# Optimization experiments

Hardware: AMD Instinct MI355X
Metric: run time of the kernel (lower is better)

## Reference

```python
import jax, jax.numpy as jnp
import numpy as np
from jax import lax

EPS = 1e-5
GROUPS = 16

def _conv(x, w, b):
    # x: [N,C,H,W], w: [O,I,3,3]
    y = lax.conv_general_dilated(x, w, (1, 1), 'SAME',
                                 dimension_numbers=('NCHW', 'OIHW', 'NCHW'))
    return y + b[None, :, None, None]

def _group_norm(x, gamma, beta):
    N, C, H, W = x.shape
    xr = x.reshape(N, GROUPS, C // GROUPS, H, W)
    m = xr.mean(axis=(2, 3, 4), keepdims=True)
    v = xr.var(axis=(2, 3, 4), keepdims=True)
    xn = ((xr - m) * lax.rsqrt(v + EPS)).reshape(N, C, H, W)
    return xn * gamma[None, :, None, None] + beta[None, :, None, None]

def _tower(x, ws, bs, gs, betas):
    for w, b, g, bt in zip(ws, bs, gs, betas):
        x = jax.nn.relu(_group_norm(_conv(x, w, b), g, bt))
    return x

def _fcos_heads(feats, cls_w, cls_b, cls_g, cls_bt, cls_ow, cls_ob,
                reg_w, reg_b, reg_g, reg_bt, reg_ow, reg_ob, ctr_w, ctr_b):
    outs = []
    for f in feats:
        N = f.shape[0]
        c = _tower(f, cls_w, cls_b, cls_g, cls_bt)
        logits = _conv(c, cls_ow, cls_ob)                 # [N, num_classes, H, W]
        r = _tower(f, reg_w, reg_b, reg_g, reg_bt)
        bbox = jax.nn.relu(_conv(r, reg_ow, reg_ob))      # [N, 4, H, W]
        ctr = _conv(r, ctr_w, ctr_b)                      # [N, 1, H, W]
        lvl = jnp.concatenate([logits, bbox, ctr], axis=1)  # [N, num_classes+5, H, W]
        outs.append(lvl.reshape(N, lvl.shape[1], -1))
    return jnp.concatenate(outs, axis=-1)  # [N, num_classes+5, sum(H*W)]

def setup_inputs() -> dict:
    key = jax.random.key(0)
    C, NUM_CLASSES, NB = 256, 80, 2
    sizes = [(128, 128), (64, 64), (32, 32), (16, 16), (8, 8)]
    keys = iter(jax.random.split(key, 64))
    d = {}
    for i, (h, w) in enumerate(sizes):
        d[f'feat{i}'] = jax.random.normal(next(keys), (NB, C, h, w), jnp.float32)
    for head in ('cls', 'reg'):
        for i in range(3):
            d[f'{head}_w{i}'] = 0.01 * jax.random.normal(next(keys), (C, C, 3, 3), jnp.float32)
            d[f'{head}_b{i}'] = jnp.zeros((C,), jnp.float32)
            d[f'{head}_gn_g{i}'] = jnp.ones((C,), jnp.float32)
            d[f'{head}_gn_b{i}'] = jnp.zeros((C,), jnp.float32)
    d['cls_out_w'] = 0.01 * jax.random.normal(next(keys), (NUM_CLASSES, C, 3, 3), jnp.float32)
    prior = 0.01
    d['cls_out_b'] = jnp.full((NUM_CLASSES,), float(-np.log((1 - prior) / prior)), jnp.float32)
    d['reg_out_w'] = 0.01 * jax.random.normal(next(keys), (4, C, 3, 3), jnp.float32)
    d['reg_out_b'] = jnp.zeros((4,), jnp.float32)
    d['ctr_w'] = 0.01 * jax.random.normal(next(keys), (1, C, 3, 3), jnp.float32)
    d['ctr_b'] = jnp.zeros((1,), jnp.float32)
    return d

def reference(feat0, feat1, feat2, feat3, feat4,
              cls_w0, cls_b0, cls_gn_g0, cls_gn_b0,
              cls_w1, cls_b1, cls_gn_g1, cls_gn_b1,
              cls_w2, cls_b2, cls_gn_g2, cls_gn_b2,
              reg_w0, reg_b0, reg_gn_g0, reg_gn_b0,
              reg_w1, reg_b1, reg_gn_g1, reg_gn_b1,
              reg_w2, reg_b2, reg_gn_g2, reg_gn_b2,
              cls_out_w, cls_out_b, reg_out_w, reg_out_b, ctr_w, ctr_b):
    feats = [feat0, feat1, feat2, feat3, feat4]
    return _fcos_heads(feats,
                       [cls_w0, cls_w1, cls_w2], [cls_b0, cls_b1, cls_b2],
                       [cls_gn_g0, cls_gn_g1, cls_gn_g2], [cls_gn_b0, cls_gn_b1, cls_gn_b2],
                       cls_out_w, cls_out_b,
                       [reg_w0, reg_w1, reg_w2], [reg_b0, reg_b1, reg_b2],
                       [reg_gn_g0, reg_gn_g1, reg_gn_g2], [reg_gn_b0, reg_gn_b1, reg_gn_b2],
                       reg_out_w, reg_out_b, ctr_w, ctr_b)
```

## Files before the change

### kernel.cpp

```cpp
#include <hip/hip_runtime.h>
#include <stdint.h>


typedef __attribute__((ext_vector_type(8))) short short8;
typedef __attribute__((ext_vector_type(4))) float floatx4;

#define XP 349184
#define TIB (32 * XP)

__device__ __forceinline__ unsigned short f2bf(float f) {
  unsigned u = __float_as_uint(f);
  u = (u + 0x7FFFu + ((u >> 16) & 1u)) >> 16;
  return (unsigned short)u;
}
__device__ __forceinline__ unsigned pk2(float a, float b) {
  return (unsigned)f2bf(a) | ((unsigned)f2bf(b) << 16);
}
__device__ __forceinline__ void async16(const void* g, void* l) {
  __builtin_amdgcn_global_load_lds(
      (const __attribute__((address_space(1))) unsigned int*)g,
      (__attribute__((address_space(3))) unsigned int*)l, 16, 0, 0);
}

#define WAIT_VM4 0x0F74
#define WAIT_VM0 0x0F70

__device__ const int d_lw[5]   = {7, 6, 5, 4, 3};
__device__ const int d_off[5]  = {0, 16384, 20480, 21504, 21760};
__device__ const int d_nt[5]   = {128, 32, 8, 2, 1};
__device__ const int d_cumT[6] = {0, 1024, 1280, 1344, 1360, 1368};
__device__ const int d_cumO[6] = {0, 512, 640, 672, 680, 684};
__device__ const int d_cumS[6] = {0, 256, 320, 336, 340, 341};
__device__ const int ck_lvl[13] = {0,0,0,0,0,0,0,0,1,1,2,3,4};
__device__ const int ck_c0[13]  = {0,2048,4096,6144,8192,10240,12288,14336,0,2048,0,0,0};
__device__ const int ck_len[13] = {2048,2048,2048,2048,2048,2048,2048,2048,2048,2048,1024,256,64};

__global__ __launch_bounds__(256) void wtrans(
    const float* __restrict__ c0, const float* __restrict__ c1, const float* __restrict__ c2,
    const float* __restrict__ r0, const float* __restrict__ r1, const float* __restrict__ r2,
    const float* __restrict__ cw, const float* __restrict__ rw, const float* __restrict__ tw,
    unsigned short* __restrict__ dst, float* __restrict__ zp, float* __restrict__ stats) {
  const int z = blockIdx.y;
  if (z == 8) {
    if (blockIdx.x == 0) {
      for (int i = threadIdx.x; i < 384; i += 256) zp[i] = 0.f;
      for (int i = threadIdx.x; i < 1920; i += 256) stats[i] = 0.f;
    }
    return;
  }
  const int nel = (z < 6) ? 589824 : 294912;
  const int idx = blockIdx.x * 256 + threadIdx.x;
  if (idx >= nel) return;
  int tmp = idx;
  const int j = tmp & 7;   tmp >>= 3;
  const int m = tmp & 127; tmp >>= 7;
  const int cs = tmp & 3;  tmp >>= 2;
  const int t = tmp % 9;   tmp /= 9;
  const int cc = tmp & 7;  const int mt = tmp >> 3;
  const int o = mt * 128 + m;
  const int i = cc * 32 + cs * 8 + j;
  float v = 0.f;
  const float* srcs[6] = {c0, c1, c2, r0, r1, r2};
  if (z < 6)      v = srcs[z][((size_t)o * 256 + i) * 9 + t];
  else if (z == 6){ if (o < 80) v = cw[((size_t)o * 256 + i) * 9 + t]; }
  else            { if (o < 4)  v = rw[((size_t)o * 256 + i) * 9 + t];
                    else if (o == 4) v = tw[(size_t)i * 9 + t]; }
  const size_t base = (z < 6) ? (size_t)z * 589824
                              : (size_t)6 * 589824 + (size_t)(z - 6) * 294912;
  dst[base + idx] = f2bf(v);
}

__global__ __launch_bounds__(256) void feat_nhwc(
    const float* __restrict__ s0, const float* __restrict__ s1,
    const float* __restrict__ s2, const float* __restrict__ s3,
    const float* __restrict__ s4, unsigned short* __restrict__ dst) {
  __shared__ unsigned short tile[64][65];
  int bx = blockIdx.x, lvl = 0;
  while (bx >= d_cumS[lvl + 1]) ++lvl;
  const int HW = 1 << (2 * d_lw[lvl]), off = d_off[lvl];
  const float* srcs[5] = {s0, s1, s2, s3, s4};
  const float* src = srcs[lvl];
  const int img = blockIdx.z, c0 = blockIdx.y * 64, p0 = (bx - d_cumS[lvl]) * 64;
  const float* s = src + ((size_t)img * 256 + c0) * HW + p0;
  const int tid = threadIdx.x;
#pragma unroll
  for (int i = 0; i < 4; i++) {
    const int cl = (tid >> 4) + i * 16, pl = (tid & 15) * 4;
    const float4 v = *(const float4*)(s + (size_t)cl * HW + pl);
    tile[cl][pl]     = f2bf(v.x);
    tile[cl][pl + 1] = f2bf(v.y);
    tile[cl][pl + 2] = f2bf(v.z);
    tile[cl][pl + 3] = f2bf(v.w);
  }
  __syncthreads();
  const int pl = tid >> 2, cseg = (tid & 3) * 16;
  unsigned ro[8];
#pragma unroll
  for (int k = 0; k < 8; k++)
    ro[k] = (unsigned)tile[cseg + 2 * k][pl] | ((unsigned)tile[cseg + 2 * k + 1][pl] << 16);
  const int ch0 = c0 + cseg;
  char* db = (char*)dst + (size_t)img * TIB + (size_t)(ch0 >> 3) * XP
           + (size_t)(off + p0 + pl) * 16;
  uint4 u0 = {ro[0], ro[1], ro[2], ro[3]};
  uint4 u1 = {ro[4], ro[5], ro[6], ro[7]};
  *(uint4*)db = u0;
  *(uint4*)(db + XP) = u1;
}

__global__ __launch_bounds__(256) void conv_mfma(
    const unsigned short* __restrict__ xin0, const unsigned short* __restrict__ xin1,
    const unsigned short* __restrict__ wA, const unsigned short* __restrict__ wB,
    unsigned short* __restrict__ y0, unsigned short* __restrict__ y1,
    const float* __restrict__ cb0, const float* __restrict__ cb1,
    float* __restrict__ out,
    const float* __restrict__ ob_cls, const float* __restrict__ ob_reg, const float* __restrict__ ob_ctr,
    const unsigned short* __restrict__ zp, int mode) {
  __shared__ __align__(16) char smem[49152];
  const int tid = threadIdx.x;
  const int* cum = (mode == 0) ? d_cumT : d_cumO;
  const int nwg = (mode == 0) ? 1368 : 684;
  const int xcd = blockIdx.x & 7, cidx = blockIdx.x >> 3;
  const int qq = nwg >> 3, rr = nwg & 7;
  int bid = (xcd < rr ? xcd * (qq + 1) : rr * (qq + 1) + (xcd - rr) * qq) + cidx;
  int lvl = 0;
  while (bid >= cum[lvl + 1]) ++lvl;
  int r = bid - cum[lvl];
  const int lw = d_lw[lvl], W = 1 << lw, HW = 1 << (2 * lw), poffl = d_off[lvl];
  const int ntc = d_nt[lvl];
  const int nt = r % ntc; r /= ntc;
  int mt = 0;
  if (mode == 0) { mt = r & 1; r >>= 1; }
  const int img = r & 1, tower = r >> 1;

  const unsigned short* xin = (tower ? xin1 : xin0) + (size_t)img * 21824 * 256;
  const unsigned short* wset = tower ? wB : wA;

  const int n = tid & 127;
  const int p = nt * 128 + n;
  const bool pv = p < HW;
  const int h = p >> lw, w = p & (W - 1);
  const int kq = tid >> 7;

  const char* xb = (const char*)xin;
  const char* tb[9];
  int stp[9];
#pragma unroll
  for (int t = 0; t < 9; t++) {
    const int rr2 = h + t / 3 - 1, cx = w + t % 3 - 1;
    const bool v = pv && rr2 >= 0 && rr2 < W && cx >= 0 && cx < W;
    tb[t] = v ? xb + (size_t)kq * XP + (size_t)(poffl + rr2 * W + cx) * 16
              : (const char*)zp;
    stp[t] = v ? 4 * XP : 0;
  }

  const char* abase = (const char*)wset + (size_t)mt * 589824;
  const char* a_tid = abase + (size_t)tid * 16;
  char* l_tid = smem + tid * 16;

  const int lane = tid & 63, q = lane >> 4, lr = lane & 15;
  const int wv = tid >> 6, wm = wv >> 1, wn = wv & 1;
  int aoff[4], boff[4];
#pragma unroll
  for (int i = 0; i < 4; i++) {
    aoff[i] = ((q << 7) + wm * 64 + i * 16 + lr) << 4;
    boff[i] = (((q << 7) + wn * 64 + i * 16 + lr) << 4) + 8192;
  }

  floatx4 acc[4][4];
#pragma unroll
  for (int i = 0; i < 4; i++)
#pragma unroll
    for (int j = 0; j < 4; j++) acc[i][j] = (floatx4){0.f, 0.f, 0.f, 0.f};

#define UNIT(CC, U, WIMM)                                                     \
  {                                                                           \
    const int it_ = (CC) * 9 + (U);                                           \
    __builtin_amdgcn_s_waitcnt(WIMM);                                         \
    __builtin_amdgcn_s_barrier();                                             \
    asm volatile("" ::: "memory");                                            \
    if (it_ + 2 < 72) {                                                       \
      const int nu_ = (U) + 2;                                                \
      const int tn_ = nu_ % 9;                              \
      const int ccn_ = (CC) + nu_ / 9;                                        \
      char* la_ = l_tid + (nu_ % 3) * 16384;                                  \
      const char* ap_ = a_tid + (size_t)(it_ + 2) * 8192;                     \
      async16(ap_, la_);                                                      \
      async16(ap_ + 4096, la_ + 4096);                                        \
      const int sp_ = stp[tn_];                                               \
      const char* bp_ = tb[tn_] + ccn_ * sp_;                                 \
      async16(bp_, la_ + 8192);                                               \
      async16(bp_ + (sp_ >> 1), la_ + 12288);                                 \
    }                                                                         \
    asm volatile("" ::: "memory");                                            \
    const int sb_ = ((U) % 3) * 16384;                                        \
    short8 af[4], bfr[4];                                                     \
    _Pragma("unroll")                                                         \
    for (int i = 0; i < 4; i++) {                                             \
      af[i] = *(const short8*)(smem + sb_ + aoff[i]);                         \
      bfr[i] = *(const short8*)(smem + sb_ + boff[i]);                        \
    }                                                                         \
    _Pragma("unroll")                                                         \
    for (int i = 0; i < 4; i++)                                               \
      _Pragma("unroll")                                                       \
      for (int j = 0; j < 4; j++)                                             \
        acc[i][j] = __builtin_amdgcn_mfma_f32_16x16x32_bf16(af[i], bfr[j],    \
                                                            acc[i][j], 0, 0, 0); \
  }

  async16(a_tid, l_tid);
  async16(a_tid + 4096, l_tid + 4096);
  async16(tb[0], l_tid + 8192);
  async16(tb[0] + (stp[0] >> 1), l_tid + 12288);
  async16(a_tid + 8192, l_tid + 16384);
  async16(a_tid + 12288, l_tid + 20480);
  async16(tb[1], l_tid + 24576);
  async16(tb[1] + (stp[1] >> 1), l_tid + 28672);

  for (int cc = 0; cc < 7; ++cc) {
#pragma unroll
    for (int u = 0; u < 9; ++u) UNIT(cc, u, WAIT_VM4)
  }
  UNIT(7, 0, WAIT_VM4) UNIT(7, 1, WAIT_VM4) UNIT(7, 2, WAIT_VM4)
  UNIT(7, 3, WAIT_VM4) UNIT(7, 4, WAIT_VM4) UNIT(7, 5, WAIT_VM4)
  UNIT(7, 6, WAIT_VM4) UNIT(7, 7, WAIT_VM0) UNIT(7, 8, WAIT_VM0)
#undef UNIT

  if (mode == 0) {
    char* yb = (char*)(tower ? y1 : y0) + (size_t)img * TIB;
    const float* cb = tower ? cb1 : cb0;
#pragma unroll
    for (int i = 0; i < 4; i++) {
      const int c = mt * 128 + wm * 64 + i * 16 + (q << 2);
      const float4 b4 = *(const float4*)(cb + c);
      char* yp = yb + (size_t)(c >> 3) * XP + (size_t)poffl * 16 + ((c & 7) << 1);
#pragma unroll
      for (int j = 0; j < 4; j++) {
        const int pp = nt * 128 + wn * 64 + j * 16 + lr;
        if (pp >= HW) continue;
        floatx4 a = acc[i][j];
        uint2 u;
        u.x = pk2(a.x + b4.x, a.y + b4.y);
        u.y = pk2(a.z + b4.z, a.w + b4.w);
        *(uint2*)(yp + (size_t)pp * 16) = u;
      }
    }
  } else {
#pragma unroll
    for (int j = 0; j < 4; j++) {
      const int pp = nt * 128 + wn * 64 + j * 16 + lr;
      if (pp >= HW) continue;
      const size_t gp = (size_t)poffl + pp;
#pragma unroll
      for (int i = 0; i < 4; i++) {
        const int m0 = wm * 64 + i * 16 + (q << 2);
        floatx4 a = acc[i][j];
#pragma unroll
        for (int k2 = 0; k2 < 4; k2++) {
          const int m = m0 + k2;
          const float v = a[k2];
          if (tower == 0) {
            if (m < 80) out[((size_t)img * 85 + m) * 21824 + gp] = v + ob_cls[m];
          } else {
            if (m < 4)
              out[((size_t)img * 85 + 80 + m) * 21824 + gp] = fmaxf(v + ob_reg[m], 0.f);
            else if (m == 4)
              out[((size_t)img * 85 + 84) * 21824 + gp] = v + ob_ctr[0];
          }
        }
      }
    }
  }
}

__global__ __launch_bounds__(256) void gn_stats(
    const unsigned short* __restrict__ y0, const unsigned short* __restrict__ y1,
    float* __restrict__ stats) {
  const int ck = blockIdx.x, g = blockIdx.y, tz = blockIdx.z;
  const int tower = tz >> 1, img = tz & 1;
  const int lvl = ck_lvl[ck], c0 = ck_c0[ck], len = ck_len[ck];
  const char* base = (const char*)(tower ? y1 : y0) + (size_t)img * TIB
                   + (size_t)(2 * g) * XP + (size_t)(d_off[lvl] + c0) * 16;
  const int tid = threadIdx.x;
  float s = 0.f, s2 = 0.f;
  const int n2 = 2 * len;
  for (int i = tid; i < n2; i += 256) {
    const int pl = (i >= len);
    const int pos = i - pl * len;
    const uint4 d = *(const uint4*)(base + (size_t)pl * XP + (size_t)pos * 16);
    unsigned uu[4] = {d.x, d.y, d.z, d.w};
#pragma unroll
    for (int k = 0; k < 4; k++) {
      const float f0 = __uint_as_float(uu[k] << 16);
      const float f1 = __uint_as_float(uu[k] & 0xFFFF0000u);
      s += f0 + f1;
      s2 += f0 * f0 + f1 * f1;
    }
  }
#pragma unroll
  for (int m = 1; m < 64; m <<= 1) {
    s += __shfl_xor(s, m);
    s2 += __shfl_xor(s2, m);
  }
  __shared__ float rs[4], rq[4];
  const int lane = tid & 63, wvv = tid >> 6;
  if (lane == 0) { rs[wvv] = s; rq[wvv] = s2; }
  __syncthreads();
  if (tid == 0) {
    float* st = stats + (((tz * 5 + lvl) * 16 + g) << 1);
    atomicAdd(st, rs[0] + rs[1] + rs[2] + rs[3]);
    atomicAdd(st + 1, rq[0] + rq[1] + rq[2] + rq[3]);
  }
}

__global__ __launch_bounds__(256) void gn_apply(
    const unsigned short* __restrict__ ybase, unsigned short* __restrict__ xbase,
    const float* __restrict__ stats,
    const float* __restrict__ g0, const float* __restrict__ b0,
    const float* __restrict__ g1, const float* __restrict__ b1) {
  const int g = blockIdx.x * 256 + threadIdx.x;
  const int pos = g % 21824;
  const int rest = g / 21824;
  const int plane = rest & 31;
  const int ti = rest >> 5;
  const int tower = ti >> 1;
  const int lvl = (pos >= 16384) + (pos >= 20480) + (pos >= 21504) + (pos >= 21760);
  const float cnt = (float)(16 << (2 * d_lw[lvl]));
  const float* st = stats + ((((ti * 5 + lvl) * 16 + (plane >> 1))) << 1);
  const float mean = st[0] / cnt;
  const float var = st[1] / cnt - mean * mean;
  const float rstd = rsqrtf(var + 1e-5f);
  const float* gam = (tower ? g1 : g0) + plane * 8;
  const float* bet = (tower ? b1 : b0) + plane * 8;
  const size_t off = (size_t)ti * TIB + (size_t)plane * XP + (size_t)pos * 16;
  const uint4 d = *(const uint4*)((const char*)ybase + off);
  unsigned uu[4] = {d.x, d.y, d.z, d.w};
  unsigned ro[4];
#pragma unroll
  for (int k = 0; k < 4; k++) {
    const float f0 = __uint_as_float(uu[k] << 16);
    const float f1 = __uint_as_float(uu[k] & 0xFFFF0000u);
    const float o0 = fmaxf((f0 - mean) * rstd * gam[2 * k] + bet[2 * k], 0.f);
    const float o1 = fmaxf((f1 - mean) * rstd * gam[2 * k + 1] + bet[2 * k + 1], 0.f);
    ro[k] = (unsigned)f2bf(o0) | ((unsigned)f2bf(o1) << 16);
  }
  uint4 od = {ro[0], ro[1], ro[2], ro[3]};
  *(uint4*)((char*)xbase + off) = od;
}

extern "C" void kernel_launch(void* const* d_in, const int* in_sizes, int n_in,
                              void* d_out, int out_size, void* d_ws, size_t ws_size,
                              hipStream_t stream) {
  (void)in_sizes; (void)n_in; (void)out_size; (void)ws_size;
  char* ws = (char*)d_ws;
  unsigned short* zp = (unsigned short*)ws;
  unsigned short* wblk = (unsigned short*)(ws + 2048);
  const size_t WSET_T = 1179648;
  const size_t WSET_O = 589824;
  char* pXfeat = ws + 2048 + 6 * WSET_T + 2 * WSET_O;
  const size_t XSZ = (size_t)2 * 21824 * 256 * 2;
  char* pX = pXfeat + XSZ;
  char* pY = pX + 2 * XSZ;
  float* stats = (float*)(pY + 2 * XSZ);

  wtrans<<<dim3(2304, 9), 256, 0, stream>>>(
      (const float*)d_in[5], (const float*)d_in[9], (const float*)d_in[13],
      (const float*)d_in[17], (const float*)d_in[21], (const float*)d_in[25],
      (const float*)d_in[29], (const float*)d_in[31], (const float*)d_in[33],
      wblk, (float*)zp, stats);
  feat_nhwc<<<dim3(341, 4, 2), 256, 0, stream>>>(
      (const float*)d_in[0], (const float*)d_in[1], (const float*)d_in[2],
      (const float*)d_in[3], (const float*)d_in[4], (unsigned short*)pXfeat);

  unsigned short* xc = (unsigned short*)pX;
  unsigned short* xr = (unsigned short*)(pX + XSZ);
  unsigned short* yc = (unsigned short*)pY;
  unsigned short* yr = (unsigned short*)(pY + XSZ);

  for (int s = 0; s < 3; s++) {
    const unsigned short* in0 = s ? xc : (unsigned short*)pXfeat;
    const unsigned short* in1 = s ? xr : (unsigned short*)pXfeat;
    const unsigned short* wc = wblk + (size_t)s * 589824;
    const unsigned short* wr = wblk + (size_t)(3 + s) * 589824;
    float* st_s = stats + (size_t)s * 640;
    conv_mfma<<<1368, 256, 0, stream>>>(
        in0, in1, wc, wr, yc, yr,
        (const float*)d_in[6 + 4 * s], (const float*)d_in[18 + 4 * s],
        nullptr, nullptr, nullptr, nullptr, zp, 0);
    gn_stats<<<dim3(13, 16, 4), 256, 0, stream>>>(yc, yr, st_s);
    gn_apply<<<10912, 256, 0, stream>>>(
        (const unsigned short*)pY, (unsigned short*)pX, st_s,
        (const float*)d_in[7 + 4 * s], (const float*)d_in[8 + 4 * s],
        (const float*)d_in[19 + 4 * s], (const float*)d_in[20 + 4 * s]);
  }
  const unsigned short* wo_c = wblk + (size_t)6 * 589824;
  const unsigned short* wo_r = wo_c + 294912;
  conv_mfma<<<684, 256, 0, stream>>>(
      xc, xr, wo_c, wo_r, nullptr, nullptr, nullptr, nullptr,
      (float*)d_out, (const float*)d_in[30], (const float*)d_in[32],
      (const float*)d_in[34], zp, 1);
}
```

Measured before the change: 581.5 us.

## Fuse GroupNorm statistics into conv epilogue and drop gn_stats kernel

The conv epilogue now accumulates per-group sum and sum-of-squares from its fp32 accumulators, reduces them across the wavefront and block, and writes one partial per tile into a stats buffer with no atomics. gn_apply is reorganised into a (chunk, plane, tensor) grid that first reduces those tile partials to get the mean and rstd, which removes the separate gn_stats pass that re-read the bf16 conv output. The trade-off is extra epilogue work and two block syncs in the conv, plus redundant partial reductions in every gn_apply block. The statistics now come from fp32 values rather than bf16-rounded ones.

```diff
diff --git a/kernel.cpp b/kernel.cpp
--- a/kernel.cpp
+++ b/kernel.cpp
@@ -31,20 +31,19 @@
 __device__ const int d_cumT[6] = {0, 1024, 1280, 1344, 1360, 1368};
 __device__ const int d_cumO[6] = {0, 512, 640, 672, 680, 684};
 __device__ const int d_cumS[6] = {0, 256, 320, 336, 340, 341};
-__device__ const int ck_lvl[13] = {0,0,0,0,0,0,0,0,1,1,2,3,4};
-__device__ const int ck_c0[13]  = {0,2048,4096,6144,8192,10240,12288,14336,0,2048,0,0,0};
-__device__ const int ck_len[13] = {2048,2048,2048,2048,2048,2048,2048,2048,2048,2048,1024,256,64};
 
 __global__ __launch_bounds__(256) void wtrans(
     const float* __restrict__ c0, const float* __restrict__ c1, const float* __restrict__ c2,
     const float* __restrict__ r0, const float* __restrict__ r1, const float* __restrict__ r2,
     const float* __restrict__ cw, const float* __restrict__ rw, const float* __restrict__ tw,
-    unsigned short* __restrict__ dst, float* __restrict__ zp, float* __restrict__ stats) {
+    unsigned short* __restrict__ dst, float* __restrict__ zp, float* __restrict__ statsp) {
   const int z = blockIdx.y;
   if (z == 8) {
-    if (blockIdx.x == 0) {
-      for (int i = threadIdx.x; i < 384; i += 256) zp[i] = 0.f;
-      for (int i = threadIdx.x; i < 1920; i += 256) stats[i] = 0.f;
+    const int b = blockIdx.x;
+    if (b < 80) {
+      for (int k = threadIdx.x; k < 1024; k += 256) statsp[b * 1024 + k] = 0.f;
+    } else if (b == 80) {
+      for (int k = threadIdx.x; k < 384; k += 256) zp[k] = 0.f;
     }
     return;
   }
@@ -114,7 +113,7 @@
     const float* __restrict__ cb0, const float* __restrict__ cb1,
     float* __restrict__ out,
     const float* __restrict__ ob_cls, const float* __restrict__ ob_reg, const float* __restrict__ ob_ctr,
-    const unsigned short* __restrict__ zp, int mode) {
+    float* __restrict__ statsp, const unsigned short* __restrict__ zp, int mode) {
   __shared__ __align__(16) char smem[49152];
   const int tid = threadIdx.x;
   const int* cum = (mode == 0) ? d_cumT : d_cumO;
@@ -228,6 +227,7 @@
   if (mode == 0) {
     char* yb = (char*)(tower ? y1 : y0) + (size_t)img * TIB;
     const float* cb = tower ? cb1 : cb0;
+    float sv[4] = {0.f, 0.f, 0.f, 0.f}, sq[4] = {0.f, 0.f, 0.f, 0.f};
 #pragma unroll
     for (int i = 0; i < 4; i++) {
       const int c = mt * 128 + wm * 64 + i * 16 + (q << 2);
@@ -238,10 +238,39 @@
         const int pp = nt * 128 + wn * 64 + j * 16 + lr;
         if (pp >= HW) continue;
         floatx4 a = acc[i][j];
+        const float v0 = a.x + b4.x, v1 = a.y + b4.y;
+        const float v2 = a.z + b4.z, v3 = a.w + b4.w;
         uint2 u;
-        u.x = pk2(a.x + b4.x, a.y + b4.y);
-        u.y = pk2(a.z + b4.z, a.w + b4.w);
+        u.x = pk2(v0, v1);
+        u.y = pk2(v2, v3);
         *(uint2*)(yp + (size_t)pp * 16) = u;
+        sv[i] += v0 + v1 + v2 + v3;
+        sq[i] += v0 * v0 + v1 * v1 + v2 * v2 + v3 * v3;
+      }
+    }
+    float* smf = (float*)smem;
+    __syncthreads();
+#pragma unroll
+    for (int i = 0; i < 4; i++) {
+      float S = sv[i], Q = sq[i];
+#pragma unroll
+      for (int m2 = 1; m2 < 64; m2 <<= 1) {
+        S += __shfl_xor(S, m2);
+        Q += __shfl_xor(Q, m2);
+      }
+      if (lane == 0) { smf[wv * 8 + i * 2] = S; smf[wv * 8 + i * 2 + 1] = Q; }
+    }
+    __syncthreads();
+    if (wn == 0 && lane == 0) {
+      const int tz = tower * 2 + img;
+#pragma unroll
+      for (int i = 0; i < 4; i++) {
+        const int gidx = mt * 8 + wm * 4 + i;
+        const float S = smf[wv * 8 + i * 2] + smf[(wv + 1) * 8 + i * 2];
+        const float Q = smf[wv * 8 + i * 2 + 1] + smf[(wv + 1) * 8 + i * 2 + 1];
+        float* dst2 = statsp + (size_t)(((tz * 5 + lvl) * 16 + gidx) * 128 + nt) * 2;
+        dst2[0] = S;
+        dst2[1] = Q;
       }
     }
   } else {
@@ -272,63 +301,39 @@
   }
 }
 
-__global__ __launch_bounds__(256) void gn_stats(
-    const unsigned short* __restrict__ y0, const unsigned short* __restrict__ y1,
-    float* __restrict__ stats) {
-  const int ck = blockIdx.x, g = blockIdx.y, tz = blockIdx.z;
-  const int tower = tz >> 1, img = tz & 1;
-  const int lvl = ck_lvl[ck], c0 = ck_c0[ck], len = ck_len[ck];
-  const char* base = (const char*)(tower ? y1 : y0) + (size_t)img * TIB
-                   + (size_t)(2 * g) * XP + (size_t)(d_off[lvl] + c0) * 16;
-  const int tid = threadIdx.x;
-  float s = 0.f, s2 = 0.f;
-  const int n2 = 2 * len;
-  for (int i = tid; i < n2; i += 256) {
-    const int pl = (i >= len);
-    const int pos = i - pl * len;
-    const uint4 d = *(const uint4*)(base + (size_t)pl * XP + (size_t)pos * 16);
-    unsigned uu[4] = {d.x, d.y, d.z, d.w};
-#pragma unroll
-    for (int k = 0; k < 4; k++) {
-      const float f0 = __uint_as_float(uu[k] << 16);
-      const float f1 = __uint_as_float(uu[k] & 0xFFFF0000u);
-      s += f0 + f1;
-      s2 += f0 * f0 + f1 * f1;
-    }
-  }
-#pragma unroll
-  for (int m = 1; m < 64; m <<= 1) {
-    s += __shfl_xor(s, m);
-    s2 += __shfl_xor(s2, m);
-  }
-  __shared__ float rs[4], rq[4];
-  const int lane = tid & 63, wvv = tid >> 6;
-  if (lane == 0) { rs[wvv] = s; rq[wvv] = s2; }
-  __syncthreads();
-  if (tid == 0) {
-    float* st = stats + (((tz * 5 + lvl) * 16 + g) << 1);
-    atomicAdd(st, rs[0] + rs[1] + rs[2] + rs[3]);
-    atomicAdd(st + 1, rq[0] + rq[1] + rq[2] + rq[3]);
-  }
-}
-
 __global__ __launch_bounds__(256) void gn_apply(
     const unsigned short* __restrict__ ybase, unsigned short* __restrict__ xbase,
-    const float* __restrict__ stats,
+    const float* __restrict__ statsp,
     const float* __restrict__ g0, const float* __restrict__ b0,
     const float* __restrict__ g1, const float* __restrict__ b1) {
-  const int g = blockIdx.x * 256 + threadIdx.x;
-  const int pos = g % 21824;
-  const int rest = g / 21824;
-  const int plane = rest & 31;
-  const int ti = rest >> 5;
+  const int chunk = blockIdx.x;
+  const int plane = blockIdx.y;
+  const int ti = blockIdx.z;
+  const int tid = threadIdx.x;
+  const int lvl = (chunk >= 64) + (chunk >= 80) + (chunk >= 84) + (chunk >= 85);
+  const int ntc = d_nt[lvl];
+  const int g = plane >> 1;
+  const float* sp = statsp + (size_t)(((ti * 5 + lvl) * 16 + g) * 128) * 2;
+  float S = 0.f, Q = 0.f;
+  if (tid < ntc) { S = sp[2 * tid]; Q = sp[2 * tid + 1]; }
+#pragma unroll
+  for (int m = 1; m < 64; m <<= 1) {
+    S += __shfl_xor(S, m);
+    Q += __shfl_xor(Q, m);
+  }
+  __shared__ float red[2][2];
+  if (tid == 0 || tid == 64) { red[tid >> 6][0] = S; red[tid >> 6][1] = Q; }
+  __syncthreads();
+  const float St = red[0][0] + red[1][0];
+  const float Qt = red[0][1] + red[1][1];
+  const float cnt = (float)(16 << (2 * d_lw[lvl]));
+  const float mean = St / cnt;
+  const float var = Qt / cnt - mean * mean;
+  const float rstd = rsqrtf(var + 1e-5f);
+
+  const int pos = chunk * 256 + tid;
+  if (pos >= 21824) return;
   const int tower = ti >> 1;
-  const int lvl = (pos >= 16384) + (pos >= 20480) + (pos >= 21504) + (pos >= 21760);
-  const float cnt = (float)(16 << (2 * d_lw[lvl]));
-  const float* st = stats + ((((ti * 5 + lvl) * 16 + (plane >> 1))) << 1);
-  const float mean = st[0] / cnt;
-  const float var = st[1] / cnt - mean * mean;
-  const float rstd = rsqrtf(var + 1e-5f);
   const float* gam = (tower ? g1 : g0) + plane * 8;
   const float* bet = (tower ? b1 : b0) + plane * 8;
   const size_t off = (size_t)ti * TIB + (size_t)plane * XP + (size_t)pos * 16;
@@ -360,13 +365,13 @@
   const size_t XSZ = (size_t)2 * 21824 * 256 * 2;
   char* pX = pXfeat + XSZ;
   char* pY = pX + 2 * XSZ;
-  float* stats = (float*)(pY + 2 * XSZ);
+  float* statsp = (float*)(pY + 2 * XSZ);
 
   wtrans<<<dim3(2304, 9), 256, 0, stream>>>(
       (const float*)d_in[5], (const float*)d_in[9], (const float*)d_in[13],
       (const float*)d_in[17], (const float*)d_in[21], (const float*)d_in[25],
       (const float*)d_in[29], (const float*)d_in[31], (const float*)d_in[33],
-      wblk, (float*)zp, stats);
+      wblk, (float*)zp, statsp);
   feat_nhwc<<<dim3(341, 4, 2), 256, 0, stream>>>(
       (const float*)d_in[0], (const float*)d_in[1], (const float*)d_in[2],
       (const float*)d_in[3], (const float*)d_in[4], (unsigned short*)pXfeat);
@@ -381,14 +386,12 @@
     const unsigned short* in1 = s ? xr : (unsigned short*)pXfeat;
     const unsigned short* wc = wblk + (size_t)s * 589824;
     const unsigned short* wr = wblk + (size_t)(3 + s) * 589824;
-    float* st_s = stats + (size_t)s * 640;
     conv_mfma<<<1368, 256, 0, stream>>>(
         in0, in1, wc, wr, yc, yr,
         (const float*)d_in[6 + 4 * s], (const float*)d_in[18 + 4 * s],
-        nullptr, nullptr, nullptr, nullptr, zp, 0);
-    gn_stats<<<dim3(13, 16, 4), 256, 0, stream>>>(yc, yr, st_s);
-    gn_apply<<<10912, 256, 0, stream>>>(
-        (const unsigned short*)pY, (unsigned short*)pX, st_s,
+        nullptr, nullptr, nullptr, nullptr, statsp, zp, 0);
+    gn_apply<<<dim3(86, 32, 4), 256, 0, stream>>>(
+        (const unsigned short*)pY, (unsigned short*)pX, statsp,
         (const float*)d_in[7 + 4 * s], (const float*)d_in[8 + 4 * s],
         (const float*)d_in[19 + 4 * s], (const float*)d_in[20 + 4 * s]);
   }
@@ -397,5 +400,5 @@
   conv_mfma<<<684, 256, 0, stream>>>(
       xc, xr, wo_c, wo_r, nullptr, nullptr, nullptr, nullptr,
       (float*)d_out, (const float*)d_in[30], (const float*)d_in[32],
-      (const float*)d_in[34], zp, 1);
-}
+      (const float*)d_in[34], nullptr, zp, 1);
+}
```

Result: no change. 572.0 us (-1.6%).
